# Kernel optimization log

Measured on AMD Instinct MI355X. Metric: run time of the kernel, lower is better.

## Reference

```python
import jax, jax.numpy as jnp
import numpy as np
import math

B, T, C, H = 2, 2048, 1024, 16
HD = C // H  # head_dim = 64


def setup_inputs() -> dict:
    key = jax.random.key(0)
    ks = jax.random.split(key, 10)
    s = 1.0 / math.sqrt(C)
    x = jax.random.normal(ks[0], (B, T, C), jnp.float32)
    wq = jax.random.normal(ks[1], (C, C), jnp.float32) * s
    wk = jax.random.normal(ks[2], (C, C), jnp.float32) * s
    wv = jax.random.normal(ks[3], (C, C), jnp.float32) * s
    wo = jax.random.normal(ks[4], (C, C), jnp.float32) * s
    bq = jnp.zeros((C,), jnp.float32)
    bk = jnp.zeros((C,), jnp.float32)
    bv = jnp.zeros((C,), jnp.float32)
    bo = jnp.zeros((C,), jnp.float32)
    fractal_dim = jnp.ones((1,), jnp.float32)  # scalar fractal dimension input
    alpha = jnp.asarray(1.5, jnp.float32)
    fractal_alpha_scale = jnp.asarray(0.5, jnp.float32)
    energy_normalizer = jnp.asarray(1.0, jnp.float32)
    return {"x": x, "fractal_dim": fractal_dim, "wq": wq, "bq": bq, "wk": wk,
            "bk": bk, "wv": wv, "bv": bv, "wo": wo, "bo": bo, "alpha": alpha,
            "fractal_alpha_scale": fractal_alpha_scale,
            "energy_normalizer": energy_normalizer}


def reference(x, fractal_dim, wq, bq, wk, bk, wv, bv, wo, bo, alpha,
              fractal_alpha_scale, energy_normalizer):
    b, t, c = x.shape
    # input energy: L2 norm over channels, [b, t, 1]
    input_energy = jnp.linalg.norm(x, axis=-1, keepdims=True)
    adaptive_alpha = alpha + fractal_alpha_scale * (fractal_dim - 1.5)  # [1]

    q = (x @ wq + bq).reshape(b, t, H, HD)
    k = (x @ wk + bk).reshape(b, t, H, HD)
    v = (x @ wv + bv).reshape(b, t, H, HD)

    # per-head FFT along the time axis -> complex64
    q_fft = jnp.fft.fft(q, axis=1)
    k_fft = jnp.fft.fft(k, axis=1)
    v_fft = jnp.fft.fft(v, axis=1)

    freqs = jnp.fft.fftfreq(t).astype(jnp.float32)  # [t]
    phase = adaptive_alpha * jnp.arctan(jnp.log(jnp.abs(freqs) + 1e-10))  # [t]
    # unit-modulus complex spectral filter, broadcast [1, t, 1, 1]
    filt = jax.lax.complex(jnp.cos(phase), jnp.sin(phase))[None, :, None, None]

    qf = q_fft * filt
    kf = k_fft * filt
    vf = v_fft * filt

    # real part of complex matmul Q_f @ K_f^T, computed without complex GEMM:
    # Re(qf kf^T) = qr kr^T - qi ki^T
    inv_sqrt = np.float32(1.0 / math.sqrt(HD))
    logits = (jnp.einsum('bthd,bshd->bhts', qf.real, kf.real)
              - jnp.einsum('bthd,bshd->bhts', qf.imag, kf.imag)) * inv_sqrt
    attn = jax.nn.softmax(logits, axis=-1)  # [b, h, t, s]

    # attn is real, so Re(attn @ vf) = attn @ Re(vf); out_proj has real weights
    # so taking the real part before the projection is exact.
    attended = jnp.einsum('bhts,bshd->bthd', attn, vf.real)
    out = attended.reshape(b, t, c) @ wo + bo

    out_energy = jnp.linalg.norm(out, axis=-1, keepdims=True)
    energy_ratio = input_energy / (out_energy + 1e-8)
    return out * energy_ratio * energy_normalizer
```

## Files before the change

kernel.cpp:

```cpp
#include <hip/hip_runtime.h>
#include <math.h>


typedef _Float16 half8 __attribute__((ext_vector_type(8)));
typedef float f32x4 __attribute__((ext_vector_type(4)));
#define MFMA16 __builtin_amdgcn_mfma_f32_16x16x32_f16

__device__ inline unsigned pack_split(float v) {
    _Float16 h = (_Float16)v;
    float r = (v - (float)h) * 2048.0f;
    _Float16 l = (_Float16)r;
    union { _Float16 f; unsigned short u; } a, b;
    a.f = h; b.f = l;
    return (unsigned)a.u | ((unsigned)b.u << 16);
}
__device__ inline _Float16 lo16(unsigned u) {
    union { unsigned short s; _Float16 f; } x; x.s = (unsigned short)(u & 0xffffu); return x.f;
}
__device__ inline _Float16 hi16(unsigned u) {
    union { unsigned short s; _Float16 f; } x; x.s = (unsigned short)(u >> 16); return x.f;
}

__device__ inline void write_split(_Float16* dh, _Float16* dl, uint4 u0, uint4 u1) {
    uint4 lo, hi;
    lo.x = __builtin_amdgcn_perm(u0.y, u0.x, 0x05040100u);
    lo.y = __builtin_amdgcn_perm(u0.w, u0.z, 0x05040100u);
    lo.z = __builtin_amdgcn_perm(u1.y, u1.x, 0x05040100u);
    lo.w = __builtin_amdgcn_perm(u1.w, u1.z, 0x05040100u);
    hi.x = __builtin_amdgcn_perm(u0.y, u0.x, 0x07060302u);
    hi.y = __builtin_amdgcn_perm(u0.w, u0.z, 0x07060302u);
    hi.z = __builtin_amdgcn_perm(u1.y, u1.x, 0x07060302u);
    hi.w = __builtin_amdgcn_perm(u1.w, u1.z, 0x07060302u);
    *(uint4*)dh = lo;
    *(uint4*)dl = hi;
}

__global__ __launch_bounds__(256) void k_init_tables(
    float2* __restrict__ tw, float2* __restrict__ filt,
    const float* __restrict__ fd, const float* __restrict__ alpha,
    const float* __restrict__ fas)
{
    int i = blockIdx.x * 256 + threadIdx.x;
    double aa = (double)alpha[0] + (double)fas[0] * ((double)fd[0] - 1.5);
    if (i < 1024) {
        double ang = -2.0 * 3.14159265358979323846 * (double)i / 2048.0;
        double s, c;
        sincos(ang, &s, &c);
        tw[i] = make_float2((float)c, (float)s);
    }
    if (i < 2048) {
        double fr = (i < 1024) ? (double)i / 2048.0 : ((double)i - 2048.0) / 2048.0;
        double ph = aa * atan(log(fabs(fr) + 1e-10));
        double s, c;
        sincos(ph, &s, &c);
        filt[i] = make_float2((float)c, (float)s);
    }
}

__global__ __launch_bounds__(256) void k_prep_w(
    const float* __restrict__ W, unsigned* __restrict__ Wpk)
{
    __shared__ float tile[64][65];
    const int kb = blockIdx.x * 64, cb = blockIdx.y * 64;
    const int t = threadIdx.x, r = t >> 4, c4 = (t & 15) * 4;
#pragma unroll
    for (int i = 0; i < 4; ++i) {
        int row = r + 16 * i;
        float4 v = *(const float4*)&W[(size_t)(kb + row) * 1024 + cb + c4];
        tile[row][c4 + 0] = v.x; tile[row][c4 + 1] = v.y;
        tile[row][c4 + 2] = v.z; tile[row][c4 + 3] = v.w;
    }
    __syncthreads();
#pragma unroll
    for (int i = 0; i < 4; ++i) {
        int crow = r + 16 * i;
        uint4 o;
        o.x = pack_split(tile[c4 + 0][crow]);
        o.y = pack_split(tile[c4 + 1][crow]);
        o.z = pack_split(tile[c4 + 2][crow]);
        o.w = pack_split(tile[c4 + 3][crow]);
        *(uint4*)&Wpk[(size_t)(cb + crow) * 1024 + kb + c4] = o;
    }
}

__global__ __launch_bounds__(256) void k_prep_x(
    const float* __restrict__ x, unsigned* __restrict__ xpk)
{
    const int base = blockIdx.x * 4096 + threadIdx.x * 4;
#pragma unroll
    for (int i = 0; i < 4; ++i) {
        int idx = base + i * 1024;
        float4 v = *(const float4*)&x[idx];
        uint4 o;
        o.x = pack_split(v.x); o.y = pack_split(v.y);
        o.z = pack_split(v.z); o.w = pack_split(v.w);
        *(uint4*)&xpk[idx] = o;
    }
}

__global__ __launch_bounds__(256) void k_gemm_qkv(
    const unsigned* __restrict__ xpk, const unsigned* __restrict__ wpk,
    const float* __restrict__ bq, const float* __restrict__ bk,
    const float* __restrict__ bv,
    float* __restrict__ qT, float* __restrict__ kT, float* __restrict__ vT)
{
    __shared__ __align__(16) _Float16 Ab[8][2][64][8];
    __shared__ __align__(16) _Float16 Bb[8][2][64][8];
    const int tid = threadIdx.x;
    const int mat = blockIdx.z;
    const unsigned* Apk = wpk + (size_t)mat * 1048576;
    const float* bias = (mat == 0) ? bq : (mat == 1) ? bk : bv;
    float* outp       = (mat == 0) ? qT : (mat == 1) ? kT : vT;
    const int m0 = blockIdx.x * 128, n0 = blockIdx.y * 128;
    const int w = tid >> 6, lane = tid & 63, quad = lane >> 4, l15 = lane & 15;
    const int wm = (w & 1) * 4, wn = (w >> 1) * 4;

    const int chA = tid & 3, rA = tid >> 2;
    const int flA = (rA & 15) + 16 * chA, mtA = rA >> 4;
    const unsigned* gA0 = &Apk[(size_t)(m0 + rA) * 1024 + chA * 8];
    const unsigned* gA1 = gA0 + (size_t)64 * 1024;
    const unsigned* gB0 = &xpk[(size_t)(n0 + rA) * 1024 + chA * 8];
    const unsigned* gB1 = gB0 + (size_t)64 * 1024;

    uint4 pa0 = *(const uint4*)gA0, pa1 = *(const uint4*)(gA0 + 4);
    uint4 pa2 = *(const uint4*)gA1, pa3 = *(const uint4*)(gA1 + 4);
    uint4 pb0 = *(const uint4*)gB0, pb1 = *(const uint4*)(gB0 + 4);
    uint4 pb2 = *(const uint4*)gB1, pb3 = *(const uint4*)(gB1 + 4);

    f32x4 acc1[4][4], acc2[4][4];
    const f32x4 z4 = {0.f, 0.f, 0.f, 0.f};
#pragma unroll
    for (int i = 0; i < 4; ++i)
#pragma unroll
        for (int j = 0; j < 4; ++j) { acc1[i][j] = z4; acc2[i][j] = z4; }

    for (int k0 = 0; k0 < 1024; k0 += 32) {
        __syncthreads();
        write_split(&Ab[mtA][0][flA][0],     &Ab[mtA][1][flA][0],     pa0, pa1);
        write_split(&Ab[mtA + 4][0][flA][0], &Ab[mtA + 4][1][flA][0], pa2, pa3);
        write_split(&Bb[mtA][0][flA][0],     &Bb[mtA][1][flA][0],     pb0, pb1);
        write_split(&Bb[mtA + 4][0][flA][0], &Bb[mtA + 4][1][flA][0], pb2, pb3);
        __syncthreads();
        if (k0 < 992) {
            int kn = k0 + 32;
            pa0 = *(const uint4*)(gA0 + kn); pa1 = *(const uint4*)(gA0 + kn + 4);
            pa2 = *(const uint4*)(gA1 + kn); pa3 = *(const uint4*)(gA1 + kn + 4);
            pb0 = *(const uint4*)(gB0 + kn); pb1 = *(const uint4*)(gB0 + kn + 4);
            pb2 = *(const uint4*)(gB1 + kn); pb3 = *(const uint4*)(gB1 + kn + 4);
        }
        half8 ah[4], al[4];
#pragma unroll
        for (int mt = 0; mt < 4; ++mt) {
            ah[mt] = *(half8*)&Ab[wm + mt][0][lane][0];
            al[mt] = *(half8*)&Ab[wm + mt][1][lane][0];
        }
#pragma unroll
        for (int nt = 0; nt < 4; ++nt) {
            half8 bh = *(half8*)&Bb[wn + nt][0][lane][0];
            half8 bl = *(half8*)&Bb[wn + nt][1][lane][0];
#pragma unroll
            for (int mt = 0; mt < 4; ++mt) {
                acc1[mt][nt] = MFMA16(ah[mt], bh, acc1[mt][nt], 0, 0, 0);
                acc2[mt][nt] = MFMA16(ah[mt], bl, acc2[mt][nt], 0, 0, 0);
                acc2[mt][nt] = MFMA16(al[mt], bh, acc2[mt][nt], 0, 0, 0);
            }
        }
    }
    const int b_ = n0 >> 11, t0 = n0 & 2047;
#pragma unroll
    for (int mt = 0; mt < 4; ++mt) {
#pragma unroll
        for (int r_ = 0; r_ < 4; ++r_) {
            int m = m0 + (wm + mt) * 16 + quad * 4 + r_;
            float bs = bias[m];
            float* orow = &outp[(size_t)(b_ * 1024 + m) * 2048 + t0];
#pragma unroll
            for (int nt = 0; nt < 4; ++nt) {
                float val = acc1[mt][nt][r_] + acc2[mt][nt][r_] * (1.f / 2048.f) + bs;
                orow[(wn + nt) * 16 + l15] = val;
            }
        }
    }
}

__global__ __launch_bounds__(256) void k_fft_filter(
    float* __restrict__ qT, float* __restrict__ kT, float* __restrict__ vT,
    float* __restrict__ qiT, float* __restrict__ kiT,
    const float2* __restrict__ tw, const float2* __restrict__ filt)
{
    __shared__ float2 sf[2048];
    const int bid = blockIdx.x;
    const int mat = bid >> 11;
    const int seq = bid & 2047;
    float* base = (mat == 0) ? qT : (mat == 1) ? kT : vT;
    float* src = base + (size_t)seq * 2048;
    const int tid = threadIdx.x;

    for (int i = tid; i < 2048; i += 256) {
        int j = (int)(__brev((unsigned)i) >> 21);
        sf[j] = make_float2(src[i], 0.f);
    }
    __syncthreads();
    for (int st = 1; st <= 11; ++st) {
        const int half = 1 << (st - 1);
        const int shift = 11 - st;
        for (int u = tid; u < 1024; u += 256) {
            int pos = u & (half - 1);
            int bi = 2 * u - pos;
            float2 w = tw[pos << shift];
            float2 a = sf[bi], b = sf[bi + half];
            float tr = w.x * b.x - w.y * b.y;
            float ti = w.x * b.y + w.y * b.x;
            sf[bi]        = make_float2(a.x + tr, a.y + ti);
            sf[bi + half] = make_float2(a.x - tr, a.y - ti);
        }
        __syncthreads();
    }
    unsigned* dst_re = (unsigned*)src;
    unsigned* dst_im = (mat == 0) ? (unsigned*)(qiT + (size_t)seq * 2048)
                                  : (unsigned*)(kiT + (size_t)seq * 2048);
    for (int i = tid; i < 2048; i += 256) {
        float2 z = sf[i];
        float2 f = filt[i];
        float re = z.x * f.x - z.y * f.y;
        float im = z.x * f.y + z.y * f.x;
        if (mat == 0) {
            dst_re[i] = pack_split(0.125f * re);
            dst_im[i] = pack_split(0.125f * im);
        } else if (mat == 1) {
            dst_re[i] = pack_split(re);
            dst_im[i] = pack_split(-im);
        } else {
            dst_re[i] = pack_split(re);
        }
    }
}

__global__ __launch_bounds__(512, 2) void k_flash(
    const unsigned* __restrict__ qpk, const unsigned* __restrict__ qipk,
    const unsigned* __restrict__ kpk, const unsigned* __restrict__ kipk,
    const unsigned* __restrict__ vpk, unsigned* __restrict__ attpk)
{
    __shared__ __align__(16) _Float16 Kbuf[2][4][4][2][64][8];
    __shared__ __align__(16) _Float16 Vbuf[2][2][4][2][64][8];

    const int tid = threadIdx.x;
    const int w = tid >> 6, lane = tid & 63;
    const int quad = lane >> 4, l15 = lane & 15;
    const int p = blockIdx.x;
    const int bh = (p & 7) * 4 + (p >> 6);
    const int tb = (p >> 3) & 7;
    const size_t bc = (size_t)bh * 64;
    const int tw0 = tb * 256 + w * 16;

    half8 aqh[2][4], aql[2][4];
#pragma unroll
    for (int rg = 0; rg < 2; ++rg) {
#pragma unroll
        for (int kc = 0; kc < 4; ++kc) {
#pragma unroll
            for (int j = 0; j < 8; ++j) {
                int d = kc * 32 + quad * 8 + j;
                int t = tw0 + rg * 128 + l15;
                unsigned u = (d < 64) ? qpk[(bc + d) * 2048 + t]
                                      : qipk[(bc + d - 64) * 2048 + t];
                aqh[rg][kc][j] = lo16(u);
                aql[rg][kc][j] = hi16(u);
            }
        }
    }

    f32x4 O1[2][4], O2[2][4];
    const f32x4 zero4 = {0.f, 0.f, 0.f, 0.f};
#pragma unroll
    for (int rg = 0; rg < 2; ++rg)
#pragma unroll
        for (int nt = 0; nt < 4; ++nt) { O1[rg][nt] = zero4; O2[rg][nt] = zero4; }
    float m_[2] = {-3e38f, -3e38f};
    float l_[2] = {0.f, 0.f};

    const int sK = tid & 63;
    const int dc0 = tid >> 6;
    const int stK = sK >> 4;
    const int kcK0 = dc0 >> 2;
    const int laneK = (sK & 15) + ((dc0 & 3) << 4);
    const unsigned* kre = &kpk[(bc + dc0 * 8) * 2048 + sK];
    const unsigned* kim = &kipk[(bc + dc0 * 8) * 2048 + sK];
    const int sc2V = tid >> 8;
    const int ntV = (tid >> 6) & 3, laneV = tid & 63;
    const int dV = ntV * 16 + (laneV & 15);
    const int s0V = sc2V * 32 + (laneV >> 4) * 4;
    const unsigned* vbase = &vpk[(bc + dV) * 2048 + s0V];

    unsigned ka0, ka1, ka2, ka3, ka4, ka5, ka6, ka7;
    unsigned kb0, kb1, kb2, kb3, kb4, kb5, kb6, kb7;
    uint4 va0, va1;
    ka0 = kre[0 * 2048]; ka1 = kre[1 * 2048];
    ka2 = kre[2 * 2048]; ka3 = kre[3 * 2048];
    ka4 = kre[4 * 2048]; ka5 = kre[5 * 2048];
    ka6 = kre[6 * 2048]; ka7 = kre[7 * 2048];
    kb0 = kim[0 * 2048]; kb1 = kim[1 * 2048];
    kb2 = kim[2 * 2048]; kb3 = kim[3 * 2048];
    kb4 = kim[4 * 2048]; kb5 = kim[5 * 2048];
    kb6 = kim[6 * 2048]; kb7 = kim[7 * 2048];
    va0 = *(const uint4*)vbase;
    va1 = *(const uint4*)(vbase + 16);
    write_split(&Kbuf[0][stK][kcK0][0][laneK][0], &Kbuf[0][stK][kcK0][1][laneK][0],
                make_uint4(ka0, ka1, ka2, ka3), make_uint4(ka4, ka5, ka6, ka7));
    write_split(&Kbuf[0][stK][kcK0 + 2][0][laneK][0], &Kbuf[0][stK][kcK0 + 2][1][laneK][0],
                make_uint4(kb0, kb1, kb2, kb3), make_uint4(kb4, kb5, kb6, kb7));
    write_split(&Vbuf[0][sc2V][ntV][0][laneV][0], &Vbuf[0][sc2V][ntV][1][laneV][0],
                va0, va1);
    kre += 64; kim += 64; vbase += 64;
    ka0 = kre[0 * 2048]; ka1 = kre[1 * 2048];
    ka2 = kre[2 * 2048]; ka3 = kre[3 * 2048];
    ka4 = kre[4 * 2048]; ka5 = kre[5 * 2048];
    ka6 = kre[6 * 2048]; ka7 = kre[7 * 2048];
    kb0 = kim[0 * 2048]; kb1 = kim[1 * 2048];
    kb2 = kim[2 * 2048]; kb3 = kim[3 * 2048];
    kb4 = kim[4 * 2048]; kb5 = kim[5 * 2048];
    kb6 = kim[6 * 2048]; kb7 = kim[7 * 2048];
    va0 = *(const uint4*)vbase;
    va1 = *(const uint4*)(vbase + 16);
    __syncthreads();

    for (int it = 0; it < 32; ++it) {
        const int cur = it & 1, nxt = cur ^ 1;
        if (it < 31) {
            write_split(&Kbuf[nxt][stK][kcK0][0][laneK][0],
                        &Kbuf[nxt][stK][kcK0][1][laneK][0],
                        make_uint4(ka0, ka1, ka2, ka3), make_uint4(ka4, ka5, ka6, ka7));
            write_split(&Kbuf[nxt][stK][kcK0 + 2][0][laneK][0],
                        &Kbuf[nxt][stK][kcK0 + 2][1][laneK][0],
                        make_uint4(kb0, kb1, kb2, kb3), make_uint4(kb4, kb5, kb6, kb7));
            write_split(&Vbuf[nxt][sc2V][ntV][0][laneV][0],
                        &Vbuf[nxt][sc2V][ntV][1][laneV][0], va0, va1);
        }
        if (it < 30) {
            kre += 64; kim += 64; vbase += 64;
            ka0 = kre[0 * 2048]; ka1 = kre[1 * 2048];
            ka2 = kre[2 * 2048]; ka3 = kre[3 * 2048];
            ka4 = kre[4 * 2048]; ka5 = kre[5 * 2048];
            ka6 = kre[6 * 2048]; ka7 = kre[7 * 2048];
            kb0 = kim[0 * 2048]; kb1 = kim[1 * 2048];
            kb2 = kim[2 * 2048]; kb3 = kim[3 * 2048];
            kb4 = kim[4 * 2048]; kb5 = kim[5 * 2048];
            kb6 = kim[6 * 2048]; kb7 = kim[7 * 2048];
            va0 = *(const uint4*)vbase;
            va1 = *(const uint4*)(vbase + 16);
        }

        f32x4 S1[2][4], S2[2][4];
#pragma unroll
        for (int rg = 0; rg < 2; ++rg)
#pragma unroll
            for (int st = 0; st < 4; ++st) { S1[rg][st] = zero4; S2[rg][st] = zero4; }
        __builtin_amdgcn_s_setprio(1);
#pragma unroll
        for (int st = 0; st < 4; ++st) {
#pragma unroll
            for (int kc = 0; kc < 4; ++kc) {
                half8 khf = *(half8*)&Kbuf[cur][st][kc][0][lane][0];
                half8 klf = *(half8*)&Kbuf[cur][st][kc][1][lane][0];
#pragma unroll
                for (int rg = 0; rg < 2; ++rg) {
                    S1[rg][st] = MFMA16(khf, aqh[rg][kc], S1[rg][st], 0, 0, 0);
                    S2[rg][st] = MFMA16(klf, aqh[rg][kc], S2[rg][st], 0, 0, 0);
                    S2[rg][st] = MFMA16(khf, aql[rg][kc], S2[rg][st], 0, 0, 0);
                }
            }
        }
        __builtin_amdgcn_s_setprio(0);

        half8 pb[2][2];
#pragma unroll
        for (int rg = 0; rg < 2; ++rg) {
#pragma unroll
            for (int st = 0; st < 4; ++st)
                S1[rg][st] = S1[rg][st] + S2[rg][st] * (1.f / 2048.f);
            float mt = -3e38f;
#pragma unroll
            for (int st = 0; st < 4; ++st)
#pragma unroll
                for (int r = 0; r < 4; ++r)
                    mt = fmaxf(mt, S1[rg][st][r]);
            mt = fmaxf(mt, __shfl_xor(mt, 16));
            mt = fmaxf(mt, __shfl_xor(mt, 32));
            float mn = fmaxf(m_[rg], mt);
            float al = __expf(m_[rg] - mn);
            m_[rg] = mn;
            float rs = 0.f;
            _Float16 ph[4][4];
#pragma unroll
            for (int st = 0; st < 4; ++st)
#pragma unroll
                for (int r = 0; r < 4; ++r) {
                    float pe = __expf(S1[rg][st][r] - mn);
                    rs += pe;
                    ph[st][r] = (_Float16)pe;
                }
            rs += __shfl_xor(rs, 16);
            rs += __shfl_xor(rs, 32);
            l_[rg] = l_[rg] * al + rs;
#pragma unroll
            for (int nt = 0; nt < 4; ++nt) { O1[rg][nt] *= al; O2[rg][nt] *= al; }
#pragma unroll
            for (int sc2 = 0; sc2 < 2; ++sc2) {
                half8 t8;
                t8[0] = ph[2 * sc2][0];     t8[1] = ph[2 * sc2][1];
                t8[2] = ph[2 * sc2][2];     t8[3] = ph[2 * sc2][3];
                t8[4] = ph[2 * sc2 + 1][0]; t8[5] = ph[2 * sc2 + 1][1];
                t8[6] = ph[2 * sc2 + 1][2]; t8[7] = ph[2 * sc2 + 1][3];
                pb[rg][sc2] = t8;
            }
        }

        __builtin_amdgcn_s_setprio(1);
#pragma unroll
        for (int sc2 = 0; sc2 < 2; ++sc2) {
#pragma unroll
            for (int nt = 0; nt < 4; ++nt) {
                half8 vh = *(half8*)&Vbuf[cur][sc2][nt][0][lane][0];
                half8 vl = *(half8*)&Vbuf[cur][sc2][nt][1][lane][0];
                O1[0][nt] = MFMA16(vh, pb[0][sc2], O1[0][nt], 0, 0, 0);
                O2[0][nt] = MFMA16(vl, pb[0][sc2], O2[0][nt], 0, 0, 0);
                O1[1][nt] = MFMA16(vh, pb[1][sc2], O1[1][nt], 0, 0, 0);
                O2[1][nt] = MFMA16(vl, pb[1][sc2], O2[1][nt], 0, 0, 0);
            }
        }
        __builtin_amdgcn_s_setprio(0);

        __syncthreads();
    }

    const int b = bh >> 4, h = bh & 15;
#pragma unroll
    for (int rg = 0; rg < 2; ++rg) {
        float inv = 1.0f / l_[rg];
        int t = tw0 + rg * 128 + l15;
        size_t row = (size_t)b * 2048 + t;
#pragma unroll
        for (int nt = 0; nt < 4; ++nt) {
#pragma unroll
            for (int r = 0; r < 4; ++r) {
                float val = (O1[rg][nt][r] + O2[rg][nt][r] * (1.f / 2048.f)) * inv;
                attpk[row * 1024 + h * 64 + nt * 16 + quad * 4 + r] = pack_split(val);
            }
        }
    }
}

__global__ __launch_bounds__(256) void k_gemm_out(
    const unsigned* __restrict__ attpk, const unsigned* __restrict__ wopk,
    const float* __restrict__ bo, float* __restrict__ out)
{
    __shared__ __align__(16) _Float16 Ab[8][2][64][8];
    __shared__ __align__(16) _Float16 Bb[8][2][64][8];
    const int tid = threadIdx.x;
    const int m0 = blockIdx.x * 128, n0 = blockIdx.y * 128;
    const int w = tid >> 6, lane = tid & 63, quad = lane >> 4, l15 = lane & 15;
    const int wm = (w & 1) * 4, wn = (w >> 1) * 4;

    const int chA = tid & 3, rA = tid >> 2;
    const int flA = (rA & 15) + 16 * chA, mtA = rA >> 4;
    const unsigned* gA0 = &attpk[(size_t)(m0 + rA) * 1024 + chA * 8];
    const unsigned* gA1 = gA0 + (size_t)64 * 1024;
    const unsigned* gB0 = &wopk[(size_t)(n0 + rA) * 1024 + chA * 8];
    const unsigned* gB1 = gB0 + (size_t)64 * 1024;

    uint4 pa0 = *(const uint4*)gA0, pa1 = *(const uint4*)(gA0 + 4);
    uint4 pa2 = *(const uint4*)gA1, pa3 = *(const uint4*)(gA1 + 4);
    uint4 pb0 = *(const uint4*)gB0, pb1 = *(const uint4*)(gB0 + 4);
    uint4 pb2 = *(const uint4*)gB1, pb3 = *(const uint4*)(gB1 + 4);

    f32x4 acc1[4][4], acc2[4][4];
    const f32x4 z4 = {0.f, 0.f, 0.f, 0.f};
#pragma unroll
    for (int i = 0; i < 4; ++i)
#pragma unroll
        for (int j = 0; j < 4; ++j) { acc1[i][j] = z4; acc2[i][j] = z4; }

    for (int k0 = 0; k0 < 1024; k0 += 32) {
        __syncthreads();
        write_split(&Ab[mtA][0][flA][0],     &Ab[mtA][1][flA][0],     pa0, pa1);
        write_split(&Ab[mtA + 4][0][flA][0], &Ab[mtA + 4][1][flA][0], pa2, pa3);
        write_split(&Bb[mtA][0][flA][0],     &Bb[mtA][1][flA][0],     pb0, pb1);
        write_split(&Bb[mtA + 4][0][flA][0], &Bb[mtA + 4][1][flA][0], pb2, pb3);
        __syncthreads();
        if (k0 < 992) {
            int kn = k0 + 32;
            pa0 = *(const uint4*)(gA0 + kn); pa1 = *(const uint4*)(gA0 + kn + 4);
            pa2 = *(const uint4*)(gA1 + kn); pa3 = *(const uint4*)(gA1 + kn + 4);
            pb0 = *(const uint4*)(gB0 + kn); pb1 = *(const uint4*)(gB0 + kn + 4);
            pb2 = *(const uint4*)(gB1 + kn); pb3 = *(const uint4*)(gB1 + kn + 4);
        }
        half8 ah[4], al[4];
#pragma unroll
        for (int mt = 0; mt < 4; ++mt) {
            ah[mt] = *(half8*)&Ab[wm + mt][0][lane][0];
            al[mt] = *(half8*)&Ab[wm + mt][1][lane][0];
        }
#pragma unroll
        for (int nt = 0; nt < 4; ++nt) {
            half8 bh = *(half8*)&Bb[wn + nt][0][lane][0];
            half8 bl = *(half8*)&Bb[wn + nt][1][lane][0];
#pragma unroll
            for (int mt = 0; mt < 4; ++mt) {
                acc1[mt][nt] = MFMA16(ah[mt], bh, acc1[mt][nt], 0, 0, 0);
                acc2[mt][nt] = MFMA16(ah[mt], bl, acc2[mt][nt], 0, 0, 0);
                acc2[mt][nt] = MFMA16(al[mt], bh, acc2[mt][nt], 0, 0, 0);
            }
        }
    }
#pragma unroll
    for (int mt = 0; mt < 4; ++mt) {
#pragma unroll
        for (int r_ = 0; r_ < 4; ++r_) {
            int m = m0 + (wm + mt) * 16 + quad * 4 + r_;
            float* orow = &out[(size_t)m * 1024 + n0];
#pragma unroll
            for (int nt = 0; nt < 4; ++nt) {
                int n = (wn + nt) * 16 + l15;
                float val = acc1[mt][nt][r_] + acc2[mt][nt][r_] * (1.f / 2048.f)
                          + bo[n0 + n];
                orow[n] = val;
            }
        }
    }
}

__global__ __launch_bounds__(256) void k_norm(
    const float* __restrict__ x, float* __restrict__ out,
    const float* __restrict__ en)
{
    const int row = blockIdx.x;
    const int tid = threadIdx.x;
    const float* xr = x + (size_t)row * 1024;
    float* orow = out + (size_t)row * 1024;
    float4 xv = *(const float4*)&xr[tid * 4];
    float4 ov = *(const float4*)&orow[tid * 4];
    float ssx = xv.x * xv.x + xv.y * xv.y + xv.z * xv.z + xv.w * xv.w;
    float sso = ov.x * ov.x + ov.y * ov.y + ov.z * ov.z + ov.w * ov.w;
#pragma unroll
    for (int m = 1; m <= 32; m <<= 1) {
        ssx += __shfl_xor(ssx, m, 64);
        sso += __shfl_xor(sso, m, 64);
    }
    __shared__ float rx[4], ro[4];
    const int wid = tid >> 6;
    if ((tid & 63) == 0) { rx[wid] = ssx; ro[wid] = sso; }
    __syncthreads();
    float tsx = rx[0] + rx[1] + rx[2] + rx[3];
    float tso = ro[0] + ro[1] + ro[2] + ro[3];
    float scale = sqrtf(tsx) / (sqrtf(tso) + 1e-8f) * en[0];
    ov.x *= scale; ov.y *= scale; ov.z *= scale; ov.w *= scale;
    *(float4*)&orow[tid * 4] = ov;
}

extern "C" void kernel_launch(void* const* d_in, const int* in_sizes, int n_in,
                              void* d_out, int out_size, void* d_ws, size_t ws_size,
                              hipStream_t stream)
{
    const float* x     = (const float*)d_in[0];
    const float* fd    = (const float*)d_in[1];
    const float* wq    = (const float*)d_in[2];
    const float* bq    = (const float*)d_in[3];
    const float* wk    = (const float*)d_in[4];
    const float* bk    = (const float*)d_in[5];
    const float* wv    = (const float*)d_in[6];
    const float* bv    = (const float*)d_in[7];
    const float* wo    = (const float*)d_in[8];
    const float* bo    = (const float*)d_in[9];
    const float* alpha = (const float*)d_in[10];
    const float* fas   = (const float*)d_in[11];
    const float* en    = (const float*)d_in[12];
    float* out = (float*)d_out;
    float* ws  = (float*)d_ws;

    float* qT  = ws;
    float* kT  = ws + (size_t)1 * 4194304;
    float* vT  = ws + (size_t)2 * 4194304;
    float* qiT = ws + (size_t)3 * 4194304;
    float* kiT = ws + (size_t)4 * 4194304;
    float* att = ws + (size_t)5 * 4194304;
    float2* tw   = (float2*)(ws + (size_t)6 * 4194304);
    float2* filt = (float2*)(ws + (size_t)6 * 4194304 + 2048);

    unsigned* wqkvpk = (unsigned*)qiT;
    unsigned* xpk    = (unsigned*)att;
    unsigned* attpk  = (unsigned*)att;
    unsigned* wopk   = (unsigned*)qT;

    k_init_tables<<<8, 256, 0, stream>>>(tw, filt, fd, alpha, fas);
    k_prep_w<<<dim3(16, 16), 256, 0, stream>>>(wq, wqkvpk);
    k_prep_w<<<dim3(16, 16), 256, 0, stream>>>(wk, wqkvpk + 1048576);
    k_prep_w<<<dim3(16, 16), 256, 0, stream>>>(wv, wqkvpk + 2097152);
    k_prep_x<<<1024, 256, 0, stream>>>(x, xpk);
    k_gemm_qkv<<<dim3(8, 32, 3), 256, 0, stream>>>(xpk, wqkvpk, bq, bk, bv,
                                                   qT, kT, vT);
    k_fft_filter<<<6144, 256, 0, stream>>>(qT, kT, vT, qiT, kiT, tw, filt);
    k_flash<<<256, 512, 0, stream>>>((const unsigned*)qT, (const unsigned*)qiT,
                                     (const unsigned*)kT, (const unsigned*)kiT,
                                     (const unsigned*)vT, attpk);
    k_prep_w<<<dim3(16, 16), 256, 0, stream>>>(wo, wopk);
    k_gemm_out<<<dim3(32, 8), 256, 0, stream>>>(attpk, wopk, bo, out);
    k_norm<<<4096, 256, 0, stream>>>(x, out, en);
}
```

Baseline: 464.6 us.

## Pack two real FFTs per complex FFT, lazy softmax rescale, merge weight prep

The FFT kernel now packs two real sequences into one complex FFT and separates them using conjugate symmetry, which halves the number of FFT blocks and butterfly passes. The flash kernel skips the running-max rescale of O and l unless some row max grows by more than 8, avoiding multiplies on most tiles. Exponentials may then grow up to e^8 before rescaling, which fp16 probabilities can hold. The three Q/K/V weight-prep launches are merged into one launch with a z-dimension grid, saving launch overhead.

```diff
diff --git a/kernel.cpp b/kernel.cpp
--- a/kernel.cpp
+++ b/kernel.cpp
@@ -54,6 +54,36 @@
         double s, c;
         sincos(ph, &s, &c);
         filt[i] = make_float2((float)c, (float)s);
+    }
+}
+
+__global__ __launch_bounds__(256) void k_prep_w3(
+    const float* __restrict__ wq, const float* __restrict__ wk,
+    const float* __restrict__ wv, unsigned* __restrict__ Wpk)
+{
+    __shared__ float tile[64][65];
+    const int z = blockIdx.z;
+    const float* W = (z == 0) ? wq : (z == 1) ? wk : wv;
+    unsigned* dst = Wpk + (size_t)z * 1048576;
+    const int kb = blockIdx.x * 64, cb = blockIdx.y * 64;
+    const int t = threadIdx.x, r = t >> 4, c4 = (t & 15) * 4;
+#pragma unroll
+    for (int i = 0; i < 4; ++i) {
+        int row = r + 16 * i;
+        float4 v = *(const float4*)&W[(size_t)(kb + row) * 1024 + cb + c4];
+        tile[row][c4 + 0] = v.x; tile[row][c4 + 1] = v.y;
+        tile[row][c4 + 2] = v.z; tile[row][c4 + 3] = v.w;
+    }
+    __syncthreads();
+#pragma unroll
+    for (int i = 0; i < 4; ++i) {
+        int crow = r + 16 * i;
+        uint4 o;
+        o.x = pack_split(tile[c4 + 0][crow]);
+        o.y = pack_split(tile[c4 + 1][crow]);
+        o.z = pack_split(tile[c4 + 2][crow]);
+        o.w = pack_split(tile[c4 + 3][crow]);
+        *(uint4*)&dst[(size_t)(cb + crow) * 1024 + kb + c4] = o;
     }
 }
 
@@ -190,15 +220,17 @@
 {
     __shared__ float2 sf[2048];
     const int bid = blockIdx.x;
-    const int mat = bid >> 11;
-    const int seq = bid & 2047;
+    const int mat = bid >> 10;
+    const int pair = bid & 1023;
+    const int seq0 = pair * 2, seq1 = seq0 + 1;
     float* base = (mat == 0) ? qT : (mat == 1) ? kT : vT;
-    float* src = base + (size_t)seq * 2048;
+    float* src0 = base + (size_t)seq0 * 2048;
+    float* src1 = base + (size_t)seq1 * 2048;
     const int tid = threadIdx.x;
 
     for (int i = tid; i < 2048; i += 256) {
         int j = (int)(__brev((unsigned)i) >> 21);
-        sf[j] = make_float2(src[i], 0.f);
+        sf[j] = make_float2(src0[i], src1[i]);
     }
     __syncthreads();
     for (int st = 1; st <= 11; ++st) {
@@ -216,22 +248,29 @@
         }
         __syncthreads();
     }
-    unsigned* dst_re = (unsigned*)src;
-    unsigned* dst_im = (mat == 0) ? (unsigned*)(qiT + (size_t)seq * 2048)
-                                  : (unsigned*)(kiT + (size_t)seq * 2048);
+    unsigned* dr0 = (unsigned*)src0;
+    unsigned* dr1 = (unsigned*)src1;
+    unsigned* di0 = (mat == 0) ? (unsigned*)(qiT + (size_t)seq0 * 2048)
+                               : (unsigned*)(kiT + (size_t)seq0 * 2048);
+    unsigned* di1 = (mat == 0) ? (unsigned*)(qiT + (size_t)seq1 * 2048)
+                               : (unsigned*)(kiT + (size_t)seq1 * 2048);
     for (int i = tid; i < 2048; i += 256) {
-        float2 z = sf[i];
+        float2 z  = sf[i];
+        float2 zm = sf[(2048 - i) & 2047];
+        float Are = 0.5f * (z.x + zm.x), Aim = 0.5f * (z.y - zm.y);
+        float Bre = 0.5f * (z.y + zm.y), Bim = 0.5f * (zm.x - z.x);
         float2 f = filt[i];
-        float re = z.x * f.x - z.y * f.y;
-        float im = z.x * f.y + z.y * f.x;
+        float re0 = Are * f.x - Aim * f.y, im0 = Are * f.y + Aim * f.x;
+        float re1 = Bre * f.x - Bim * f.y, im1 = Bre * f.y + Bim * f.x;
         if (mat == 0) {
-            dst_re[i] = pack_split(0.125f * re);
-            dst_im[i] = pack_split(0.125f * im);
+            dr0[i] = pack_split(0.125f * re0); di0[i] = pack_split(0.125f * im0);
+            dr1[i] = pack_split(0.125f * re1); di1[i] = pack_split(0.125f * im1);
         } else if (mat == 1) {
-            dst_re[i] = pack_split(re);
-            dst_im[i] = pack_split(-im);
+            dr0[i] = pack_split(re0); di0[i] = pack_split(-im0);
+            dr1[i] = pack_split(re1); di1[i] = pack_split(-im1);
         } else {
-            dst_re[i] = pack_split(re);
+            dr0[i] = pack_split(re0);
+            dr1[i] = pack_split(re1);
         }
     }
 }
@@ -386,9 +425,15 @@
                     mt = fmaxf(mt, S1[rg][st][r]);
             mt = fmaxf(mt, __shfl_xor(mt, 16));
             mt = fmaxf(mt, __shfl_xor(mt, 32));
-            float mn = fmaxf(m_[rg], mt);
-            float al = __expf(m_[rg] - mn);
-            m_[rg] = mn;
+            if (!__all(mt <= m_[rg] + 8.f)) {
+                float mn2 = fmaxf(m_[rg], mt);
+                float al = __expf(m_[rg] - mn2);
+                m_[rg] = mn2;
+                l_[rg] *= al;
+#pragma unroll
+                for (int nt = 0; nt < 4; ++nt) { O1[rg][nt] *= al; O2[rg][nt] *= al; }
+            }
+            float mn = m_[rg];
             float rs = 0.f;
             _Float16 ph[4][4];
 #pragma unroll
@@ -401,9 +446,7 @@
                 }
             rs += __shfl_xor(rs, 16);
             rs += __shfl_xor(rs, 32);
-            l_[rg] = l_[rg] * al + rs;
-#pragma unroll
-            for (int nt = 0; nt < 4; ++nt) { O1[rg][nt] *= al; O2[rg][nt] *= al; }
+            l_[rg] += rs;
 #pragma unroll
             for (int sc2 = 0; sc2 < 2; ++sc2) {
                 half8 t8;
@@ -592,13 +635,11 @@
     unsigned* wopk   = (unsigned*)qT;
 
     k_init_tables<<<8, 256, 0, stream>>>(tw, filt, fd, alpha, fas);
-    k_prep_w<<<dim3(16, 16), 256, 0, stream>>>(wq, wqkvpk);
-    k_prep_w<<<dim3(16, 16), 256, 0, stream>>>(wk, wqkvpk + 1048576);
-    k_prep_w<<<dim3(16, 16), 256, 0, stream>>>(wv, wqkvpk + 2097152);
+    k_prep_w3<<<dim3(16, 16, 3), 256, 0, stream>>>(wq, wk, wv, wqkvpk);
     k_prep_x<<<1024, 256, 0, stream>>>(x, xpk);
     k_gemm_qkv<<<dim3(8, 32, 3), 256, 0, stream>>>(xpk, wqkvpk, bq, bk, bv,
                                                    qT, kT, vT);
-    k_fft_filter<<<6144, 256, 0, stream>>>(qT, kT, vT, qiT, kiT, tw, filt);
+    k_fft_filter<<<3072, 256, 0, stream>>>(qT, kT, vT, qiT, kiT, tw, filt);
     k_flash<<<256, 512, 0, stream>>>((const unsigned*)qT, (const unsigned*)qiT,
                                      (const unsigned*)kT, (const unsigned*)kiT,
                                      (const unsigned*)vT, attpk);
```

Result: faster. 439.2 us (-5.5%).
